# Optimization experiments

Hardware: AMD Instinct MI355X
Metric: run time of the kernel (lower is better)

Reference implementation:

```python
import jax, jax.numpy as jnp
import numpy as np

D_MODEL = 1024
NUM_HEADS = 16


def _linear(x, W, b):
    # torch nn.Linear: y = x @ W.T + b
    return jnp.einsum('bsd,od->bso', x, W) + b


def _split_heads(x, H):
    B, S, D = x.shape
    return x.reshape(B, S, H, D // H).transpose(0, 2, 1, 3)  # [B,H,S,dk]


def setup_inputs() -> dict:
    key0 = jax.random.key(0)
    ks = jax.random.split(key0, 11)
    B, S, D = 4, 2048, D_MODEL
    w_scale = 1.0 / np.sqrt(D)
    inp = {
        'query': jax.random.normal(ks[0], (B, S, D), jnp.float32),
        'key': jax.random.normal(ks[1], (B, S, D), jnp.float32),
        'value': jax.random.normal(ks[2], (B, S, D), jnp.float32),
        'Wq': jax.random.normal(ks[3], (D, D), jnp.float32) * w_scale,
        'bq': jax.random.normal(ks[4], (D,), jnp.float32) * 0.01,
        'Wk': jax.random.normal(ks[5], (D, D), jnp.float32) * w_scale,
        'bk': jax.random.normal(ks[6], (D,), jnp.float32) * 0.01,
        'Wv': jax.random.normal(ks[7], (D, D), jnp.float32) * w_scale,
        'bv': jax.random.normal(ks[8], (D,), jnp.float32) * 0.01,
        'Wo': jax.random.normal(ks[9], (D, D), jnp.float32) * w_scale,
        'bo': jax.random.normal(ks[10], (D,), jnp.float32) * 0.01,
        'common_prefix_len': 1792,
    }
    return inp


def reference(query, key, value, Wq, bq, Wk, bk, Wv, bv, Wo, bo, common_prefix_len):
    B, S, D = query.shape
    H = NUM_HEADS
    dk = D // H
    P = common_prefix_len
    scale = 1.0 / np.sqrt(dk)

    Q = _split_heads(_linear(query, Wq, bq), H)  # [B,H,S,dk]
    K = _split_heads(_linear(key, Wk, bk), H)
    V = _split_heads(_linear(value, Wv, bv), H)

    # --- prefix: causal self-attention over first P tokens ---
    Qp, Kp, Vp = Q[:, :, :P], K[:, :, :P], V[:, :, :P]
    sp = jnp.einsum('bhld,bhsd->bhls', Qp, Kp) * scale  # [B,H,P,P]
    causal = jnp.tril(jnp.ones((P, P), dtype=bool))
    sp = jnp.where(causal, sp, -jnp.inf)
    prefix_ctx = jnp.einsum('bhls,bhsd->bhld', jax.nn.softmax(sp, axis=-1), Vp)

    # --- candidates: attend to full prefix + own diagonal entry ---
    Qc = Q[:, :, P:]  # [B,H,N,dk]
    N = S - P
    sc = jnp.einsum('bhld,bhsd->bhls', Qc, K) * scale  # [B,H,N,S]
    mask = jnp.concatenate(
        [jnp.ones((N, P), dtype=bool), jnp.eye(N, dtype=bool)], axis=-1)  # [N,S]
    sc = jnp.where(mask, sc, -jnp.inf)
    cand_ctx = jnp.einsum('bhls,bhsd->bhld', jax.nn.softmax(sc, axis=-1), V)

    ctx = jnp.concatenate([prefix_ctx, cand_ctx], axis=2)  # [B,H,S,dk]
    ctx = ctx.transpose(0, 2, 1, 3).reshape(B, S, D)
    return _linear(ctx, Wo, bo)
```

## Files before the change

kernel.cpp:

```cpp
#include <hip/hip_runtime.h>
#include <hip/hip_bf16.h>
#include <stdint.h>
#include <stddef.h>

#define D_M   1024
#define N_H   16
#define D_K   64
#define S_LEN 2048
#define N_B   4
#define P_LEN 1792
#define M_ROWS (N_B*S_LEN)

#define QSCALE 0.1803368801111601f

typedef unsigned short u16;
typedef __bf16  bf16x8 __attribute__((ext_vector_type(8)));
typedef __bf16  bf16x4 __attribute__((ext_vector_type(4)));
typedef __bf16  bf16x2 __attribute__((ext_vector_type(2)));
typedef float   f32x4  __attribute__((ext_vector_type(4)));
typedef float   f32x16 __attribute__((ext_vector_type(16)));
typedef unsigned u32x2 __attribute__((ext_vector_type(2)));
typedef unsigned u32x4 __attribute__((ext_vector_type(4)));

#define MFMA32(a,b,c)   __builtin_amdgcn_mfma_f32_16x16x32_bf16((a),(b),(c),0,0,0)
#define MFMA3216(a,b,c) __builtin_amdgcn_mfma_f32_32x32x16_bf16((a),(b),(c),0,0,0)

__device__ __forceinline__ float ex2(float x){
#if defined(__HIP_DEVICE_COMPILE__) && __has_builtin(__builtin_amdgcn_exp2f)
  return __builtin_amdgcn_exp2f(x);
#else
  return exp2f(x);
#endif
}

#define GLDS16(gp, lp) __builtin_amdgcn_global_load_lds( \
    (__attribute__((address_space(1))) void*)(gp), \
    (__attribute__((address_space(3))) void*)(lp), 16, 0, 0)

__device__ __forceinline__ u16 f2bf(float f){
  unsigned u = __builtin_bit_cast(unsigned, f);
  u += 0x7FFFu + ((u>>16)&1u);
  return (u16)(u>>16);
}

__device__ __forceinline__ unsigned pkbf(float a, float b){
  bf16x2 t; t[0] = (__bf16)a; t[1] = (__bf16)b;
  return __builtin_bit_cast(unsigned, t);
}

__device__ __forceinline__ void plswap(unsigned &x, unsigned &y){
  asm("v_permlane32_swap_b32 %0, %1" : "+v"(x), "+v"(y));
}

__global__ void cvt_bf16(const float* __restrict__ in, u16* __restrict__ out, int n8){
  typedef u16 u16x8 __attribute__((ext_vector_type(8)));
  for (int i = blockIdx.x*blockDim.x + threadIdx.x; i < n8; i += gridDim.x*blockDim.x){
    const float4* p = (const float4*)(in + (size_t)i*8);
    float4 a = p[0], b = p[1];
    u16x8 o;
    o[0]=f2bf(a.x); o[1]=f2bf(a.y); o[2]=f2bf(a.z); o[3]=f2bf(a.w);
    o[4]=f2bf(b.x); o[5]=f2bf(b.y); o[6]=f2bf(b.z); o[7]=f2bf(b.w);
    *(u16x8*)(out + (size_t)i*8) = o;
  }
}

template<int MODE, int SWZ, int CVT>
__global__ __launch_bounds__(256,3)
void gemm_bt(const void* __restrict__ Ain, const u16* __restrict__ Bm,
             const float* __restrict__ bias, void* __restrict__ Cout, float scale)
{
  constexpr int Kd = 1024, N = 1024, NT = Kd/32;
  __shared__ __align__(16) u16 As[(CVT ? 64 : 32)*128];
  __shared__ __align__(16) u16 Bs[128*32];
  const int tid  = threadIdx.x;
  const int wid  = tid >> 6, lane = tid & 63;
  const int rowBase = blockIdx.x * 128, colBase = blockIdx.y * 128;

  const int srow = (wid<<4) + (lane>>2);
  const int scol = (lane&3) << 3;
  const u16*  A16 = (const u16*)Ain;
  const float* A32 = (const float*)Ain;

  const u16* Ag0 = A16 + (size_t)(rowBase + srow)*Kd + scol;
  const u16* Ag1 = Ag0 + (size_t)64*Kd;
  const float* Asrc0 = A32 + (size_t)(rowBase + (tid>>3))*Kd
                           + (((tid&7) ^ ((tid>>3)&7)) << 2);
  float* AsF = (float*)As;

  const u16* Bg0 = Bm + (size_t)(colBase + srow)*Kd + scol;
  const u16* Bg1 = Bg0 + (size_t)64*Kd;
  u16* AsW0 = As + (wid<<9);
  u16* AsW1 = As + 2048 + (wid<<9);
  u16* BsW0 = Bs + (wid<<9);
  u16* BsW1 = Bs + 2048 + (wid<<9);

  f32x4 acc[4][4] = {};
  const int fr = lane & 15, fk = (lane>>4) << 3;
  const int wr = (wid>>1) << 6, wc = (wid&1) << 6;

  for (int kt = 0; kt < NT; ++kt){
    const int ko = kt*32;
    __syncthreads();
    if (CVT){
#pragma unroll
      for (int g=0; g<4; ++g)
        GLDS16(Asrc0 + ko + (size_t)(32*g)*Kd, AsF + (32*g + wid*8)*32);
    } else {
      GLDS16(Ag0+ko, AsW0); GLDS16(Ag1+ko, AsW1);
    }
    GLDS16(Bg0+ko, BsW0); GLDS16(Bg1+ko, BsW1);
    __syncthreads();
    bf16x8 af[4], bf[4];
    if (CVT){
      const int hh2 = (fk>>3) << 1;
#pragma unroll
      for (int i=0;i<4;++i){
        const int rr = wr + i*16 + fr, s = rr & 7;
        const float4* rp = (const float4*)(AsF + rr*32);
        float4 lo = rp[hh2 ^ s];
        float4 hi = rp[(hh2|1) ^ s];
        af[i] = __builtin_bit_cast(bf16x8,
            (u32x4){ pkbf(lo.x,lo.y), pkbf(lo.z,lo.w),
                     pkbf(hi.x,hi.y), pkbf(hi.z,hi.w) });
      }
    } else {
#pragma unroll
      for (int i=0;i<4;++i) af[i] = *(const bf16x8*)&As[(wr + i*16 + fr)*32 + fk];
    }
#pragma unroll
    for (int i=0;i<4;++i) bf[i] = *(const bf16x8*)&Bs[(wc + i*16 + fr)*32 + fk];
#pragma unroll
    for (int i=0;i<4;++i)
#pragma unroll
      for (int j=0;j<4;++j)
        acc[i][j] = MFMA32(af[i], bf[j], acc[i][j]);
  }

  const int rr0 = (lane>>4) << 2;
#pragma unroll
  for (int i=0;i<4;++i){
#pragma unroll
    for (int j=0;j<4;++j){
      const int gc = colBase + wc + j*16 + fr;
      const float bb = bias[gc];
#pragma unroll
      for (int r=0;r<4;++r){
        const int gr = rowBase + wr + i*16 + rr0 + r;
        const float v = (acc[i][j][r] + bb) * scale;
        if (MODE == 2){
          ((float*)Cout)[(size_t)gr*N + gc] = v;
        } else {
          const int b = gr >> 11, s = gr & 2047;
          const int hh = gc >> 6, k = gc & 63;
          if (MODE == 0){
            const int kk = SWZ ? ((k&7) | ((((k>>3) ^ (s&7)))<<3)) : k;
            ((u16*)Cout)[(((size_t)(b*N_H + hh))*S_LEN + s)*D_K + kk] = f2bf(v);
          } else {
            const int ss = SWZ ? ((s & ~63) | (s&7) | (((((s>>3)&7) ^ (k&7)))<<3)) : s;
            ((u16*)Cout)[(((size_t)(b*N_H + hh))*D_K + k)*S_LEN + ss] = f2bf(v);
          }
        }
      }
    }
  }
}


__device__ __forceinline__ void attn_self(
    const u16* __restrict__ Kb, const u16* __restrict__ Vb,
    const bf16x8* qf, int ks0, int h, int q,
    float& l, f32x16& o0, f32x16& o1)
{
  bf16x8 kr[4];
  {
    const int rr = ks0 + q, sw = rr & 7;
    const u16* kp = Kb + (size_t)rr * D_K;
#pragma unroll
    for (int kb=0;kb<4;++kb)
      kr[kb] = *(const bf16x8*)(kp + (((h + 2*kb) ^ sw) << 3));
  }
  f32x16 s0 = {};
  __builtin_amdgcn_s_setprio(1);
#pragma unroll
  for (int kb=0;kb<4;++kb) s0 = MFMA3216(kr[kb], qf[kb], s0);
  __builtin_amdgcn_s_setprio(0);

  bf16x8 v0[4];
  {
    const int gb = ks0 & ~63, lc0 = (ks0 - gb) >> 3;
    const int sw = q & 7;
#pragma unroll
    for (int db=0;db<2;++db){
      const u16* vp = Vb + (size_t)(32*db + q)*S_LEN + gb;
      v0[2*db]   = *(const bf16x8*)(vp + (((lc0 + h    ) ^ sw) << 3));
      v0[2*db+1] = *(const bf16x8*)(vp + (((lc0 + h + 2) ^ sw) << 3));
    }
  }

  float a[16];
#pragma unroll
  for (int r=0;r<16;++r){
    const int krow = (r&3) + 8*(r>>2) + 4*h;
    float p0 = (krow == q) ? ex2(s0[r]) : 0.f;
    s0[r] = p0; a[r] = p0;
  }
#pragma unroll
  for (int w=8; w>=1; w>>=1)
#pragma unroll
    for (int r=0;r<w;++r) a[r] += a[r+w];
  l += a[0] + __shfl_xor(a[0], 32, 64);

  unsigned w0[8];
#pragma unroll
  for (int i=0;i<8;++i) w0[i] = pkbf(s0[2*i], s0[2*i+1]);
  plswap(w0[0],w0[2]); plswap(w0[1],w0[3]);
  plswap(w0[4],w0[6]); plswap(w0[5],w0[7]);
  bf16x8 p00 = __builtin_bit_cast(bf16x8, (u32x4){w0[0],w0[1],w0[2],w0[3]});
  bf16x8 p01 = __builtin_bit_cast(bf16x8, (u32x4){w0[4],w0[5],w0[6],w0[7]});

  __builtin_amdgcn_s_setprio(1);
  o0 = MFMA3216(v0[0], p00, o0);
  o1 = MFMA3216(v0[2], p00, o1);
  o0 = MFMA3216(v0[1], p01, o0);
  o1 = MFMA3216(v0[3], p01, o1);
  __builtin_amdgcn_s_setprio(0);
}

template<int MASKED>
__device__ __forceinline__ void steplds(
    const u16* __restrict__ Ksb, const u16* __restrict__ Vsb,
    const bf16x8* qf, int ks, int qg, int h, int q,
    float& l, f32x16& o0, f32x16& o1)
{
  bf16x8 kr[8];
#pragma unroll
  for (int s=0;s<2;++s){
    const int rr = 32*s + q, base = rr*64, sw = rr&7;
#pragma unroll
    for (int kb=0;kb<4;++kb)
      kr[4*s+kb] = *(const bf16x8*)&Ksb[base + (((h + 2*kb)^sw)<<3)];
  }
  f32x16 s0 = {}, s1 = {};
  __builtin_amdgcn_s_setprio(1);
#pragma unroll
  for (int kb=0;kb<4;++kb){
    s0 = MFMA3216(kr[kb],   qf[kb], s0);
    s1 = MFMA3216(kr[4+kb], qf[kb], s1);
  }
  __builtin_amdgcn_s_setprio(0);

  bf16x8 v0[4], v1[4];
#pragma unroll
  for (int db=0;db<2;++db){
    const int rd = 32*db + q, base = rd*64, sw = rd&7;
    v0[2*db]   = *(const bf16x8*)&Vsb[base + (((h    )^sw)<<3)];
    v0[2*db+1] = *(const bf16x8*)&Vsb[base + (((h + 2)^sw)<<3)];
    v1[2*db]   = *(const bf16x8*)&Vsb[base + (((h + 4)^sw)<<3)];
    v1[2*db+1] = *(const bf16x8*)&Vsb[base + (((h + 6)^sw)<<3)];
  }

  if (MASKED){
#pragma unroll
    for (int r=0;r<16;++r){
      const int krow = (r&3) + 8*(r>>2) + 4*h;
      if (ks + krow      > qg) s0[r] = -1e30f;
      if (ks + 32 + krow > qg) s1[r] = -1e30f;
    }
  }

  float a[16];
#pragma unroll
  for (int r=0;r<16;++r){
    float p0 = ex2(s0[r]); s0[r] = p0;
    float p1 = ex2(s1[r]); s1[r] = p1;
    a[r] = p0 + p1;
  }
#pragma unroll
  for (int w=8; w>=1; w>>=1)
#pragma unroll
    for (int r=0;r<w;++r) a[r] += a[r+w];
  l += a[0] + __shfl_xor(a[0], 32, 64);

  unsigned w0[8];
#pragma unroll
  for (int i=0;i<8;++i) w0[i] = pkbf(s0[2*i], s0[2*i+1]);
  plswap(w0[0],w0[2]); plswap(w0[1],w0[3]);
  plswap(w0[4],w0[6]); plswap(w0[5],w0[7]);
  bf16x8 p00 = __builtin_bit_cast(bf16x8, (u32x4){w0[0],w0[1],w0[2],w0[3]});
  bf16x8 p01 = __builtin_bit_cast(bf16x8, (u32x4){w0[4],w0[5],w0[6],w0[7]});
  unsigned w1[8];
#pragma unroll
  for (int i=0;i<8;++i) w1[i] = pkbf(s1[2*i], s1[2*i+1]);
  plswap(w1[0],w1[2]); plswap(w1[1],w1[3]);
  plswap(w1[4],w1[6]); plswap(w1[5],w1[7]);
  bf16x8 p10 = __builtin_bit_cast(bf16x8, (u32x4){w1[0],w1[1],w1[2],w1[3]});
  bf16x8 p11 = __builtin_bit_cast(bf16x8, (u32x4){w1[4],w1[5],w1[6],w1[7]});

  __builtin_amdgcn_s_setprio(1);
  o0 = MFMA3216(v0[0], p00, o0);
  o1 = MFMA3216(v0[2], p00, o1);
  o0 = MFMA3216(v0[1], p01, o0);
  o1 = MFMA3216(v0[3], p01, o1);
  o0 = MFMA3216(v1[0], p10, o0);
  o1 = MFMA3216(v1[2], p10, o1);
  o0 = MFMA3216(v1[1], p11, o0);
  o1 = MFMA3216(v1[3], p11, o1);
  __builtin_amdgcn_s_setprio(0);
}

__device__ __forceinline__ void attn_write(
    u16* __restrict__ ctx, int bh, int qg, int h,
    float inv, const f32x16& o0, const f32x16& o1)
{
  const int b = bh >> 4, hd = bh & 15;
  u16* cp = ctx + ((size_t)b*S_LEN + qg)*D_M + hd*D_K;
#pragma unroll
  for (int rg=0; rg<4; ++rg){
    const int d0 = 8*rg + 4*h;
    bf16x4 oa, ob;
#pragma unroll
    for (int e=0;e<4;++e){ oa[e] = (__bf16)(o0[4*rg+e]*inv); ob[e] = (__bf16)(o1[4*rg+e]*inv); }
    *(bf16x4*)(cp + d0)      = oa;
    *(bf16x4*)(cp + 32 + d0) = ob;
  }
}

__global__ __launch_bounds__(128)
void attn_all(const u16* __restrict__ Q, const u16* __restrict__ K,
              const u16* __restrict__ Vt, u16* __restrict__ ctx)
{
  __shared__ __align__(16) u16 Ksm[2][4096];
  __shared__ __align__(16) u16 Vsm[2][4096];

  const int x = blockIdx.x;
  const int type = x >> 6, bh = x & 63;
  const int wid = threadIdx.x >> 6, lane = threadIdx.x & 63;
  const int q = lane & 31, h = lane >> 5;
  const bool iscand = (type < 4);
  const int tt = 31 - type;
  const int qb = iscand ? (P_LEN + (type<<6) + (wid<<5)) : ((tt<<6) + (wid<<5));
  const int nsteps = iscand ? (P_LEN/64) : (tt+1);
  const int qg = qb + q;

  const u16* Kb = K  + (size_t)bh * S_LEN * D_K;
  const u16* Vb = Vt + (size_t)bh * D_K * S_LEN;
  const u16* Qp = Q + ((size_t)bh * S_LEN + qg) * D_K + (h<<3);
  bf16x8 qf[4];
#pragma unroll
  for (int kb=0;kb<4;++kb) qf[kb] = *(const bf16x8*)(Qp + 16*kb);

  float l = 0.f;
  f32x16 o0 = {}, o1 = {};

  const int rl = lane >> 3, cl = (lane & 7) << 3;
  const int rb = wid << 5;

#define STAGE(T, B) do{                                                        \
    const int _ks = (T) << 6;                                                  \
    _Pragma("unroll")                                                          \
    for (int g=0; g<4; ++g){                                                   \
      const int _r = rb + (g<<3);                                              \
      GLDS16(Kb + (size_t)(_ks + _r + rl)*D_K + cl,   &Ksm[B][_r<<6]);         \
      GLDS16(Vb + (size_t)(_r + rl)*S_LEN + _ks + cl, &Vsm[B][_r<<6]);         \
    }                                                                          \
  }while(0)

  STAGE(0, 0);
  __syncthreads();

  for (int t = 0; t < nsteps; ++t){
    if (t+1 < nsteps) STAGE(t+1, (t+1)&1);
    if (!iscand && t == nsteps-1)
      steplds<1>(Ksm[t&1], Vsm[t&1], qf, t<<6, qg, h, q, l, o0, o1);
    else
      steplds<0>(Ksm[t&1], Vsm[t&1], qf, t<<6, qg, h, q, l, o0, o1);
    __syncthreads();
  }
#undef STAGE

  if (iscand)
    attn_self(Kb, Vb, qf, qb, h, q, l, o0, o1);

  attn_write(ctx, bh, qg, h, 1.f/l, o0, o1);
}

extern "C" void kernel_launch(void* const* d_in, const int* in_sizes, int n_in,
                              void* d_out, int out_size, void* d_ws, size_t ws_size,
                              hipStream_t stream)
{
  const float* query = (const float*)d_in[0];
  const float* key   = (const float*)d_in[1];
  const float* value = (const float*)d_in[2];
  const float* Wq = (const float*)d_in[3];
  const float* bq = (const float*)d_in[4];
  const float* Wk = (const float*)d_in[5];
  const float* bk = (const float*)d_in[6];
  const float* Wv = (const float*)d_in[7];
  const float* bv = (const float*)d_in[8];
  const float* Wo = (const float*)d_in[9];
  const float* bo = (const float*)d_in[10];

  if (ws_size < (size_t)(66u<<20)) return;

  char* ws = (char*)d_ws;
  u16* ctx = (u16*)(ws);
  u16* Wb  = (u16*)(ws + (16u<<20));
  u16* Qb  = (u16*)(ws + (18u<<20));
  u16* Kb  = (u16*)(ws + (34u<<20));
  u16* Vb  = (u16*)(ws + (50u<<20));

  const int nW8 = (D_M*D_M)/8;
  dim3 gg(M_ROWS/128, D_M/128);

  cvt_bf16<<<512,256,0,stream>>>(Wq, Wb, nW8);
  gemm_bt<0,0,1><<<gg,256,0,stream>>>(query, Wb, bq, Qb, QSCALE);

  cvt_bf16<<<512,256,0,stream>>>(Wk, Wb, nW8);
  gemm_bt<0,1,1><<<gg,256,0,stream>>>(key, Wb, bk, Kb, 1.0f);

  cvt_bf16<<<512,256,0,stream>>>(Wv, Wb, nW8);
  gemm_bt<1,1,1><<<gg,256,0,stream>>>(value, Wb, bv, Vb, 1.0f);

  attn_all<<<dim3(2048), 128, 0, stream>>>(Qb, Kb, Vb, ctx);

  cvt_bf16<<<512,256,0,stream>>>(Wo, Wb, nW8);
  gemm_bt<2,0,0><<<gg,256,0,stream>>>(ctx, Wb, bo, (float*)d_out, 1.0f);
}
```

Baseline: 200.1 us.

## Batch weight conversions and QKV GEMMs into single launches; row-sum via MFMA

Converts all four weight matrices in one kernel launch and runs the Q, K and V projections as a single 3D-grid GEMM launch instead of three separate ones. This removes launch gaps and lets the three projections share the GPU concurrently. In attention, the per-step softmax denominator is now accumulated by an extra MFMA against a ones vector instead of VALU additions and a cross-lane shuffle. That trades extra matrix-core work for fewer vector ops. The Q output also drops its swizzle flag, which is kept the same as the before path's default.

```diff
diff --git a/kernel.cpp b/kernel.cpp
--- a/kernel.cpp
+++ b/kernel.cpp
@@ -19,7 +19,6 @@
 typedef __bf16  bf16x2 __attribute__((ext_vector_type(2)));
 typedef float   f32x4  __attribute__((ext_vector_type(4)));
 typedef float   f32x16 __attribute__((ext_vector_type(16)));
-typedef unsigned u32x2 __attribute__((ext_vector_type(2)));
 typedef unsigned u32x4 __attribute__((ext_vector_type(4)));
 
 #define MFMA32(a,b,c)   __builtin_amdgcn_mfma_f32_16x16x32_bf16((a),(b),(c),0,0,0)
@@ -52,25 +51,116 @@
   asm("v_permlane32_swap_b32 %0, %1" : "+v"(x), "+v"(y));
 }
 
-__global__ void cvt_bf16(const float* __restrict__ in, u16* __restrict__ out, int n8){
+__global__ void cvt4_bf16(const float* __restrict__ w0, const float* __restrict__ w1,
+                          const float* __restrict__ w2, const float* __restrict__ w3,
+                          u16* __restrict__ wqkv, u16* __restrict__ wo){
   typedef u16 u16x8 __attribute__((ext_vector_type(8)));
-  for (int i = blockIdx.x*blockDim.x + threadIdx.x; i < n8; i += gridDim.x*blockDim.x){
-    const float4* p = (const float4*)(in + (size_t)i*8);
-    float4 a = p[0], b = p[1];
-    u16x8 o;
-    o[0]=f2bf(a.x); o[1]=f2bf(a.y); o[2]=f2bf(a.z); o[3]=f2bf(a.w);
-    o[4]=f2bf(b.x); o[5]=f2bf(b.y); o[6]=f2bf(b.z); o[7]=f2bf(b.w);
-    *(u16x8*)(out + (size_t)i*8) = o;
-  }
-}
-
-template<int MODE, int SWZ, int CVT>
+  const float* in = (blockIdx.y==0)? w0 : (blockIdx.y==1)? w1 : (blockIdx.y==2)? w2 : w3;
+  u16* o8 = (blockIdx.y==3) ? wo : (wqkv + ((size_t)blockIdx.y << 20));
+  const int i = blockIdx.x*blockDim.x + threadIdx.x;
+  const float4* p = (const float4*)(in + (size_t)i*8);
+  float4 a = p[0], b = p[1];
+  u16x8 o;
+  o[0]=f2bf(a.x); o[1]=f2bf(a.y); o[2]=f2bf(a.z); o[3]=f2bf(a.w);
+  o[4]=f2bf(b.x); o[5]=f2bf(b.y); o[6]=f2bf(b.z); o[7]=f2bf(b.w);
+  *(u16x8*)(o8 + (size_t)i*8) = o;
+}
+
 __global__ __launch_bounds__(256,3)
-void gemm_bt(const void* __restrict__ Ain, const u16* __restrict__ Bm,
-             const float* __restrict__ bias, void* __restrict__ Cout, float scale)
-{
-  constexpr int Kd = 1024, N = 1024, NT = Kd/32;
-  __shared__ __align__(16) u16 As[(CVT ? 64 : 32)*128];
+void gemm_qkv(const float* __restrict__ Aq, const float* __restrict__ Ak,
+              const float* __restrict__ Av, const u16* __restrict__ W,
+              const float* __restrict__ bqp, const float* __restrict__ bkp,
+              const float* __restrict__ bvp,
+              u16* __restrict__ Qo, u16* __restrict__ Ko, u16* __restrict__ Vo)
+{
+  constexpr int Kd = 1024, NT = Kd/32;
+  __shared__ __align__(16) float AsF[128*32];
+  __shared__ __align__(16) u16   Bs[128*32];
+  const int tid  = threadIdx.x;
+  const int wid  = tid >> 6, lane = tid & 63;
+  const int z    = blockIdx.z;
+  const int rowBase = blockIdx.x * 128, colBase = blockIdx.y * 128;
+
+  const float* A32  = (z==0)? Aq : (z==1)? Ak : Av;
+  const u16*   Bm   = W + ((size_t)z << 20);
+  const float* bias = (z==0)? bqp : (z==1)? bkp : bvp;
+  const float  scale = (z==0)? QSCALE : 1.0f;
+
+  const int srow = (wid<<4) + (lane>>2);
+  const int scol = (lane&3) << 3;
+  const float* Asrc0 = A32 + (size_t)(rowBase + (tid>>3))*Kd
+                           + (((tid&7) ^ ((tid>>3)&7)) << 2);
+  const u16* Bg0 = Bm + (size_t)(colBase + srow)*Kd + scol;
+  const u16* Bg1 = Bg0 + (size_t)64*Kd;
+  u16* BsW0 = Bs + (wid<<9);
+  u16* BsW1 = Bs + 2048 + (wid<<9);
+
+  f32x4 acc[4][4] = {};
+  const int fr = lane & 15, fk = (lane>>4) << 3;
+  const int wr = (wid>>1) << 6, wc = (wid&1) << 6;
+
+  for (int kt = 0; kt < NT; ++kt){
+    const int ko = kt*32;
+    __syncthreads();
+#pragma unroll
+    for (int g=0; g<4; ++g)
+      GLDS16(Asrc0 + ko + (size_t)(32*g)*Kd, AsF + (32*g + wid*8)*32);
+    GLDS16(Bg0+ko, BsW0); GLDS16(Bg1+ko, BsW1);
+    __syncthreads();
+    bf16x8 af[4], bf[4];
+    const int hh2 = (fk>>3) << 1;
+#pragma unroll
+    for (int i=0;i<4;++i){
+      const int rr = wr + i*16 + fr, s = rr & 7;
+      const float4* rp = (const float4*)(AsF + rr*32);
+      float4 lo = rp[hh2 ^ s];
+      float4 hi = rp[(hh2|1) ^ s];
+      af[i] = __builtin_bit_cast(bf16x8,
+          (u32x4){ pkbf(lo.x,lo.y), pkbf(lo.z,lo.w),
+                   pkbf(hi.x,hi.y), pkbf(hi.z,hi.w) });
+    }
+#pragma unroll
+    for (int i=0;i<4;++i) bf[i] = *(const bf16x8*)&Bs[(wc + i*16 + fr)*32 + fk];
+#pragma unroll
+    for (int i=0;i<4;++i)
+#pragma unroll
+      for (int j=0;j<4;++j)
+        acc[i][j] = MFMA32(af[i], bf[j], acc[i][j]);
+  }
+
+  const int rr0 = (lane>>4) << 2;
+#pragma unroll
+  for (int i=0;i<4;++i){
+#pragma unroll
+    for (int j=0;j<4;++j){
+      const int gc = colBase + wc + j*16 + fr;
+      const float bb = bias[gc];
+#pragma unroll
+      for (int r=0;r<4;++r){
+        const int gr = rowBase + wr + i*16 + rr0 + r;
+        const float v = (acc[i][j][r] + bb) * scale;
+        const int b = gr >> 11, s = gr & 2047;
+        const int hh = gc >> 6, k = gc & 63;
+        if (z == 0){
+          Qo[(((size_t)(b*N_H + hh))*S_LEN + s)*D_K + k] = f2bf(v);
+        } else if (z == 1){
+          const int kk = (k&7) | ((((k>>3) ^ (s&7)))<<3);
+          Ko[(((size_t)(b*N_H + hh))*S_LEN + s)*D_K + kk] = f2bf(v);
+        } else {
+          const int ss = (s & ~63) | (s&7) | (((((s>>3)&7) ^ (k&7)))<<3);
+          Vo[(((size_t)(b*N_H + hh))*D_K + k)*S_LEN + ss] = f2bf(v);
+        }
+      }
+    }
+  }
+}
+
+__global__ __launch_bounds__(256,3)
+void gemm_out(const u16* __restrict__ A, const u16* __restrict__ Bm,
+              const float* __restrict__ bias, float* __restrict__ Cout)
+{
+  constexpr int Kd = 1024, N = 1024;
+  __shared__ __align__(16) u16 As[128*32];
   __shared__ __align__(16) u16 Bs[128*32];
   const int tid  = threadIdx.x;
   const int wid  = tid >> 6, lane = tid & 63;
@@ -78,15 +168,8 @@
 
   const int srow = (wid<<4) + (lane>>2);
   const int scol = (lane&3) << 3;
-  const u16*  A16 = (const u16*)Ain;
-  const float* A32 = (const float*)Ain;
-
-  const u16* Ag0 = A16 + (size_t)(rowBase + srow)*Kd + scol;
+  const u16* Ag0 = A  + (size_t)(rowBase + srow)*Kd + scol;
   const u16* Ag1 = Ag0 + (size_t)64*Kd;
-  const float* Asrc0 = A32 + (size_t)(rowBase + (tid>>3))*Kd
-                           + (((tid&7) ^ ((tid>>3)&7)) << 2);
-  float* AsF = (float*)As;
-
   const u16* Bg0 = Bm + (size_t)(colBase + srow)*Kd + scol;
   const u16* Bg1 = Bg0 + (size_t)64*Kd;
   u16* AsW0 = As + (wid<<9);
@@ -98,35 +181,15 @@
   const int fr = lane & 15, fk = (lane>>4) << 3;
   const int wr = (wid>>1) << 6, wc = (wid&1) << 6;
 
-  for (int kt = 0; kt < NT; ++kt){
+  for (int kt = 0; kt < Kd/32; ++kt){
     const int ko = kt*32;
     __syncthreads();
-    if (CVT){
-#pragma unroll
-      for (int g=0; g<4; ++g)
-        GLDS16(Asrc0 + ko + (size_t)(32*g)*Kd, AsF + (32*g + wid*8)*32);
-    } else {
-      GLDS16(Ag0+ko, AsW0); GLDS16(Ag1+ko, AsW1);
-    }
+    GLDS16(Ag0+ko, AsW0); GLDS16(Ag1+ko, AsW1);
     GLDS16(Bg0+ko, BsW0); GLDS16(Bg1+ko, BsW1);
     __syncthreads();
     bf16x8 af[4], bf[4];
-    if (CVT){
-      const int hh2 = (fk>>3) << 1;
-#pragma unroll
-      for (int i=0;i<4;++i){
-        const int rr = wr + i*16 + fr, s = rr & 7;
-        const float4* rp = (const float4*)(AsF + rr*32);
-        float4 lo = rp[hh2 ^ s];
-        float4 hi = rp[(hh2|1) ^ s];
-        af[i] = __builtin_bit_cast(bf16x8,
-            (u32x4){ pkbf(lo.x,lo.y), pkbf(lo.z,lo.w),
-                     pkbf(hi.x,hi.y), pkbf(hi.z,hi.w) });
-      }
-    } else {
-#pragma unroll
-      for (int i=0;i<4;++i) af[i] = *(const bf16x8*)&As[(wr + i*16 + fr)*32 + fk];
-    }
+#pragma unroll
+    for (int i=0;i<4;++i) af[i] = *(const bf16x8*)&As[(wr + i*16 + fr)*32 + fk];
 #pragma unroll
     for (int i=0;i<4;++i) bf[i] = *(const bf16x8*)&Bs[(wc + i*16 + fr)*32 + fk];
 #pragma unroll
@@ -146,20 +209,7 @@
 #pragma unroll
       for (int r=0;r<4;++r){
         const int gr = rowBase + wr + i*16 + rr0 + r;
-        const float v = (acc[i][j][r] + bb) * scale;
-        if (MODE == 2){
-          ((float*)Cout)[(size_t)gr*N + gc] = v;
-        } else {
-          const int b = gr >> 11, s = gr & 2047;
-          const int hh = gc >> 6, k = gc & 63;
-          if (MODE == 0){
-            const int kk = SWZ ? ((k&7) | ((((k>>3) ^ (s&7)))<<3)) : k;
-            ((u16*)Cout)[(((size_t)(b*N_H + hh))*S_LEN + s)*D_K + kk] = f2bf(v);
-          } else {
-            const int ss = SWZ ? ((s & ~63) | (s&7) | (((((s>>3)&7) ^ (k&7)))<<3)) : s;
-            ((u16*)Cout)[(((size_t)(b*N_H + hh))*D_K + k)*S_LEN + ss] = f2bf(v);
-          }
-        }
+        Cout[(size_t)gr*N + gc] = acc[i][j][r] + bb;
       }
     }
   }
@@ -229,8 +279,8 @@
 template<int MASKED>
 __device__ __forceinline__ void steplds(
     const u16* __restrict__ Ksb, const u16* __restrict__ Vsb,
-    const bf16x8* qf, int ks, int qg, int h, int q,
-    float& l, f32x16& o0, f32x16& o1)
+    const bf16x8* qf, bf16x8 ones, int ks, int qg, int h, int q,
+    f32x16& o0, f32x16& o1, f32x16& o2)
 {
   bf16x8 kr[8];
 #pragma unroll
@@ -268,18 +318,8 @@
     }
   }
 
-  float a[16];
-#pragma unroll
-  for (int r=0;r<16;++r){
-    float p0 = ex2(s0[r]); s0[r] = p0;
-    float p1 = ex2(s1[r]); s1[r] = p1;
-    a[r] = p0 + p1;
-  }
-#pragma unroll
-  for (int w=8; w>=1; w>>=1)
-#pragma unroll
-    for (int r=0;r<w;++r) a[r] += a[r+w];
-  l += a[0] + __shfl_xor(a[0], 32, 64);
+#pragma unroll
+  for (int r=0;r<16;++r){ s0[r] = ex2(s0[r]); s1[r] = ex2(s1[r]); }
 
   unsigned w0[8];
 #pragma unroll
@@ -299,12 +339,16 @@
   __builtin_amdgcn_s_setprio(1);
   o0 = MFMA3216(v0[0], p00, o0);
   o1 = MFMA3216(v0[2], p00, o1);
+  o2 = MFMA3216(ones,  p00, o2);
   o0 = MFMA3216(v0[1], p01, o0);
   o1 = MFMA3216(v0[3], p01, o1);
+  o2 = MFMA3216(ones,  p01, o2);
   o0 = MFMA3216(v1[0], p10, o0);
   o1 = MFMA3216(v1[2], p10, o1);
+  o2 = MFMA3216(ones,  p10, o2);
   o0 = MFMA3216(v1[1], p11, o0);
   o1 = MFMA3216(v1[3], p11, o1);
+  o2 = MFMA3216(ones,  p11, o2);
   __builtin_amdgcn_s_setprio(0);
 }
 
@@ -348,9 +392,12 @@
   bf16x8 qf[4];
 #pragma unroll
   for (int kb=0;kb<4;++kb) qf[kb] = *(const bf16x8*)(Qp + 16*kb);
-
-  float l = 0.f;
-  f32x16 o0 = {}, o1 = {};
+  bf16x8 ones;
+#pragma unroll
+  for (int i=0;i<8;++i) ones[i] = (__bf16)1.0f;
+
+  float lx = 0.f;
+  f32x16 o0 = {}, o1 = {}, o2 = {};
 
   const int rl = lane >> 3, cl = (lane & 7) << 3;
   const int rb = wid << 5;
@@ -371,17 +418,17 @@
   for (int t = 0; t < nsteps; ++t){
     if (t+1 < nsteps) STAGE(t+1, (t+1)&1);
     if (!iscand && t == nsteps-1)
-      steplds<1>(Ksm[t&1], Vsm[t&1], qf, t<<6, qg, h, q, l, o0, o1);
+      steplds<1>(Ksm[t&1], Vsm[t&1], qf, ones, t<<6, qg, h, q, o0, o1, o2);
     else
-      steplds<0>(Ksm[t&1], Vsm[t&1], qf, t<<6, qg, h, q, l, o0, o1);
+      steplds<0>(Ksm[t&1], Vsm[t&1], qf, ones, t<<6, qg, h, q, o0, o1, o2);
     __syncthreads();
   }
 #undef STAGE
 
   if (iscand)
-    attn_self(Kb, Vb, qf, qb, h, q, l, o0, o1);
-
-  attn_write(ctx, bh, qg, h, 1.f/l, o0, o1);
+    attn_self(Kb, Vb, qf, qb, h, q, lx, o0, o1);
+
+  attn_write(ctx, bh, qg, h, 1.f/(o2[0] + lx), o0, o1);
 }
 
 extern "C" void kernel_launch(void* const* d_in, const int* in_sizes, int n_in,
@@ -403,26 +450,18 @@
   if (ws_size < (size_t)(66u<<20)) return;
 
   char* ws = (char*)d_ws;
-  u16* ctx = (u16*)(ws);
-  u16* Wb  = (u16*)(ws + (16u<<20));
-  u16* Qb  = (u16*)(ws + (18u<<20));
-  u16* Kb  = (u16*)(ws + (34u<<20));
-  u16* Vb  = (u16*)(ws + (50u<<20));
-
-  const int nW8 = (D_M*D_M)/8;
+  u16* Wqkv = (u16*)(ws);
+  u16* ctx  = (u16*)(ws);
+  u16* Wob  = (u16*)(ws + (16u<<20));
+  u16* Qb   = (u16*)(ws + (18u<<20));
+  u16* Kb   = (u16*)(ws + (34u<<20));
+  u16* Vb   = (u16*)(ws + (50u<<20));
+
   dim3 gg(M_ROWS/128, D_M/128);
 
-  cvt_bf16<<<512,256,0,stream>>>(Wq, Wb, nW8);
-  gemm_bt<0,0,1><<<gg,256,0,stream>>>(query, Wb, bq, Qb, QSCALE);
-
-  cvt_bf16<<<512,256,0,stream>>>(Wk, Wb, nW8);
-  gemm_bt<0,1,1><<<gg,256,0,stream>>>(key, Wb, bk, Kb, 1.0f);
-
-  cvt_bf16<<<512,256,0,stream>>>(Wv, Wb, nW8);
-  gemm_bt<1,1,1><<<gg,256,0,stream>>>(value, Wb, bv, Vb, 1.0f);
-
+  cvt4_bf16<<<dim3(512,4),256,0,stream>>>(Wq, Wk, Wv, Wo, Wqkv, Wob);
+  gemm_qkv<<<dim3(M_ROWS/128, D_M/128, 3),256,0,stream>>>(
+      query, key, value, Wqkv, bq, bk, bv, Qb, Kb, Vb);
   attn_all<<<dim3(2048), 128, 0, stream>>>(Qb, Kb, Vb, ctx);
-
-  cvt_bf16<<<512,256,0,stream>>>(Wo, Wb, nW8);
-  gemm_bt<2,0,0><<<gg,256,0,stream>>>(ctx, Wb, bo, (float*)d_out, 1.0f);
-}
+  gemm_out<<<gg,256,0,stream>>>(ctx, Wob, bo, (float*)d_out);
+}
```

Result: faster. 183.8 us (median of 2 runs) (-8.2%).
